# Performance work log

Hardware: AMD Instinct MI355X
Metric: run time of the kernel (lower is better)

The kernel has to match this reference:

```python
import jax, jax.numpy as jnp
import numpy as np


def setup_inputs() -> dict:
    key = jax.random.key(0)
    k1, k2, k3, k4 = jax.random.split(key, 4)
    d_in, d_out = 1024, 1024
    x = jax.random.normal(k1, (4, 2048, d_in), dtype=jnp.float32)
    # nn.Linear weights, stored as [d_in, d_out] for x @ W (torch stores transpose)
    s = 1.0 / np.sqrt(d_in)
    Wq = jax.random.normal(k2, (d_in, d_out), dtype=jnp.float32) * s
    Wk = jax.random.normal(k3, (d_in, d_out), dtype=jnp.float32) * s
    Wv = jax.random.normal(k4, (d_in, d_out), dtype=jnp.float32) * s
    return {"x": x, "Wq": Wq, "Wk": Wk, "Wv": Wv}


def reference(x, Wq, Wk, Wv):
    # x: [b, s, d_in]; projections (no bias)
    q = jnp.einsum('bsi,io->bso', x, Wq)
    k = jnp.einsum('bsi,io->bso', x, Wk)
    v = jnp.einsum('bsi,io->bso', x, Wv)
    d_out = k.shape[-1]
    scores = jnp.einsum('bqd,bkd->bqk', q, k) / jnp.sqrt(jnp.float32(d_out))
    seq_len = x.shape[1]
    causal = jnp.tril(jnp.ones((seq_len, seq_len), dtype=bool))  # [s, s]
    scores = jnp.where(causal[None, :, :], scores, -jnp.inf)
    weights = jax.nn.softmax(scores, axis=-1)
    return jnp.einsum('bqk,bkd->bqd', weights, v)
```

## Files before the change

kernel.cpp:

```cpp
#include <hip/hip_runtime.h>

typedef __attribute__((ext_vector_type(8))) short bf16x8;
typedef __attribute__((ext_vector_type(4))) float f32x4;
typedef unsigned int u32;

__device__ __forceinline__ unsigned short f2bf(float f) {
  union { float f; unsigned int u; } a; a.f = f;
  unsigned int u = a.u;
  u += 0x7FFFu + ((u >> 16) & 1u);
  return (unsigned short)(u >> 16);
}

__device__ __forceinline__ void gload16(const unsigned short* g, unsigned short* l) {
  __builtin_amdgcn_global_load_lds((const __attribute__((address_space(1))) u32*)g,
                                   (__attribute__((address_space(3))) u32*)l, 16, 0, 0);
}

#define BK 64

template<int MODE>
__global__ __launch_bounds__(256, 4)
void gemm_bt(const unsigned short* __restrict__ A,
             const unsigned short* __restrict__ Bm,
             float* __restrict__ Cf,
             float* __restrict__ Cf2,
             unsigned short* __restrict__ Cb,
             int K, long aBatch, long bBatch, long cBatch, float scale)
{
  constexpr int NI    = 2;
  constexpr int BROWS = 16;
  constexpr int BG    = 2;

  int z = blockIdx.z;
  A  += (long)z * aBatch;
  Bm += (long)z * bBatch;
  if (MODE == 2) { Cb += (long)z * cBatch; Cf += (long)z * 2048; }
  if (MODE == 3) { Cf += (long)z * cBatch; Cf2 += (long)z * 2048; }

  int bm0 = 0, bn, p = 0;
  if (MODE == 2) {
    int f = blockIdx.x;
    int r = (int)((sqrtf((float)(4 * f + 1)) - 1.0f) * 0.5f);
    while ((r + 1) * (r + 2) <= f) r++;
    while (r * (r + 1) > f) r--;
    bm0 = r * 128;
    bn  = (f - r * (r + 1)) * 64;
  } else if (MODE == 3) {
    p  = blockIdx.y;
    bn = blockIdx.x * 64;
  } else {
    bm0 = blockIdx.y * 128;
    bn  = blockIdx.x * 64;
  }

  __shared__ __align__(16) unsigned short As[128 * BK];
  __shared__ __align__(16) unsigned short Bs[64 * BK];

  int tid  = threadIdx.x;
  int wave = tid >> 6, lane = tid & 63;
  int wm = wave * 32, wn = 0;
  int quad = lane >> 4, l16 = lane & 15;

  int r8 = lane >> 3;
  int c  = (lane & 7) ^ r8;
  const unsigned short* Bg = Bm + (long)(bn + wave * BROWS + r8) * K + c * 8;
  unsigned short* Al = &As[(wave * 32) * BK];
  unsigned short* Bl = &Bs[(wave * BROWS) * BK];

  const int nseg = (MODE == 3) ? 2 : 1;
  for (int seg = 0; seg < nseg; seg++) {
    int bm   = (MODE == 3) ? ((seg == 0) ? (15 - p) * 128 : p * 128) : bm0;
    int Keff = (MODE == 3) ? ((seg == 0) ? 128 * (16 - p) : 128 * (p + 1)) : K;
    const unsigned short* Ag = A + (long)(bm + wave * 32 + r8) * K + c * 8;

    f32x4 acc[NI][4] = {};

    for (int k0 = 0; k0 < Keff; k0 += BK) {
#pragma unroll
      for (int g = 0; g < 4; g++)
        gload16(Ag + k0 + (long)g * 8 * K, Al + g * 8 * BK);
#pragma unroll
      for (int g = 0; g < BG; g++)
        gload16(Bg + k0 + (long)g * 8 * K, Bl + g * 8 * BK);
      __syncthreads();

#pragma unroll
      for (int h = 0; h < 2; h++) {
        bf16x8 af[NI], bfr[4];
#pragma unroll
        for (int i = 0; i < NI; i++)
          af[i]  = *(const bf16x8*)&As[(wm + i * 16 + l16) * BK + (((quad + 4 * h) ^ (l16 & 7)) * 8)];
#pragma unroll
        for (int j = 0; j < 4; j++)
          bfr[j] = *(const bf16x8*)&Bs[(wn + j * 16 + l16) * BK + (((quad + 4 * h) ^ (l16 & 7)) * 8)];
#pragma unroll
        for (int i = 0; i < NI; i++)
#pragma unroll
          for (int j = 0; j < 4; j++)
            acc[i][j] = __builtin_amdgcn_mfma_f32_16x16x32_bf16(af[i], bfr[j], acc[i][j], 0, 0, 0);
      }
      __syncthreads();
    }

#pragma unroll
    for (int i = 0; i < NI; i++) {
      int grow0 = bm + wm + i * 16 + quad * 4;
      if (MODE == 2) {
#pragma unroll
        for (int r = 0; r < 4; r++) {
          int grow = grow0 + r;
          float rowpart = 0.f;
#pragma unroll
          for (int j = 0; j < 4; j++) {
            int gcol = bn + j * 16 + l16;
            float e = (gcol <= grow) ? __expf(acc[i][j][r] * scale) : 0.f;
            rowpart += e;
            Cb[(long)grow * 2048 + gcol] = f2bf(e);
          }
          rowpart += __shfl_xor(rowpart, 1);
          rowpart += __shfl_xor(rowpart, 2);
          rowpart += __shfl_xor(rowpart, 4);
          rowpart += __shfl_xor(rowpart, 8);
          if (l16 == 0) atomicAdd(&Cf[grow], rowpart);
        }
      } else if (MODE == 3) {
        float rinv[4];
#pragma unroll
        for (int r = 0; r < 4; r++) rinv[r] = 1.0f / Cf2[grow0 + r];
#pragma unroll
        for (int j = 0; j < 4; j++) {
          int gcol = bn + j * 16 + l16;
#pragma unroll
          for (int r = 0; r < 4; r++)
            Cf[(long)(grow0 + r) * 1024 + gcol] = acc[i][j][r] * rinv[r];
        }
      } else {
#pragma unroll
        for (int j = 0; j < 4; j++) {
          int gcol = bn + j * 16 + l16;
#pragma unroll
          for (int r = 0; r < 4; r++)
            Cb[(long)(grow0 + r) * 1024 + gcol] = f2bf(acc[i][j][r]);
        }
      }
    }
  }
}

__global__ __launch_bounds__(512, 2)
void gemm_tv8(const unsigned short* __restrict__ A,
              const unsigned short* __restrict__ Bm,
              unsigned short* __restrict__ Cb)
{
  constexpr int NT = 16;
  constexpr int SLOT = 256 * 64;
  __shared__ __align__(16) unsigned short AsL[2 * SLOT];
  __shared__ __align__(16) unsigned short BsL[2 * SLOT];

  const int tid  = threadIdx.x;
  const int wave = tid >> 6, lane = tid & 63;
  const int quad = lane >> 4, l16 = lane & 15;
  const int wr = wave >> 2, wc = wave & 3;
  const int bm = blockIdx.y * 256;
  const int bn = blockIdx.x * 256;

  const int l8 = lane >> 3;
  const int sc = ((lane & 7) ^ l8) * 8;
  const unsigned short* Ag = A  + (long)(bm + wave * 8 + l8) * 1024 + sc;
  const unsigned short* Bg = Bm + (long)(bn + (wave >> 2) * 64 + (wave & 3) * 8 + l8) * 1024 + sc;

#define STGA(base, h, t) {                                                      \
    gload16(Ag + (long)((h) * 64) * 1024 + (t) * 64,        (base) + ((h) * 128 + wave * 8) * 64);      \
    gload16(Ag + (long)(128 + (h) * 64) * 1024 + (t) * 64,  (base) + ((h) * 128 + 64 + wave * 8) * 64); }
#define STGB(base, h, t) {                                                      \
    gload16(Bg + (long)((h) * 32) * 1024 + (t) * 64,        (base) + ((h) * 128 + wave * 8) * 64);      \
    gload16(Bg + (long)(128 + (h) * 32) * 1024 + (t) * 64,  (base) + ((h) * 128 + 64 + wave * 8) * 64); }

#define RD_A(afX, src, qm) _Pragma("unroll") for (int i = 0; i < 4; ++i)        \
    _Pragma("unroll") for (int h2 = 0; h2 < 2; ++h2)                            \
      afX[i][h2] = *(const bf16x8*)&(src)[((qm) * 128 + wr * 64 + i * 16 + l16) * 64 + (((quad + 4 * h2) ^ (l16 & 7)) * 8)];
#define RD_B(bfX, src, qn) _Pragma("unroll") for (int j = 0; j < 2; ++j)        \
    _Pragma("unroll") for (int h2 = 0; h2 < 2; ++h2)                            \
      bfX[j][h2] = *(const bf16x8*)&(src)[((qn) * 128 + wc * 32 + j * 16 + l16) * 64 + (((quad + 4 * h2) ^ (l16 & 7)) * 8)];
#define MFMA16(afX, bfX, MI0, NJ0) {                                            \
    __builtin_amdgcn_s_setprio(1);                                              \
    _Pragma("unroll") for (int i = 0; i < 4; ++i)                               \
      _Pragma("unroll") for (int j = 0; j < 2; ++j)                             \
        _Pragma("unroll") for (int h2 = 0; h2 < 2; ++h2)                        \
          acc[(MI0) + i][(NJ0) + j] =                                           \
            __builtin_amdgcn_mfma_f32_16x16x32_bf16(afX[i][h2], bfX[j][h2], acc[(MI0) + i][(NJ0) + j], 0, 0, 0); \
    __builtin_amdgcn_s_setprio(0); }

  f32x4 acc[8][4] = {};

  STGA(AsL, 0, 0) STGB(BsL, 0, 0)
  STGA(AsL, 1, 0) STGB(BsL, 1, 0)
  STGB(BsL + SLOT, 0, 1) STGA(AsL + SLOT, 1, 1)
  asm volatile("s_waitcnt vmcnt(4)" ::: "memory");
  __builtin_amdgcn_sched_barrier(0);
  __builtin_amdgcn_s_barrier();

#pragma unroll 1
  for (int u = 0; u < NT; ++u) {
    const int b = u & 1;
    const unsigned short* Asb = AsL + b * SLOT;
    const unsigned short* Bsb = BsL + b * SLOT;
    unsigned short* Asn = AsL + (b ^ 1) * SLOT;
    unsigned short* Bsn = BsL + (b ^ 1) * SLOT;
    unsigned short* Asc = AsL + b * SLOT;
    unsigned short* Bsc = BsL + b * SLOT;

    bf16x8 af0[4][2], af1[4][2], bf0[2][2], bf1[2][2];

    RD_A(af0, Asb, 0)
    RD_B(bf0, Bsb, 0)
    if (u + 1 < NT) { STGA(Asn, 0, u + 1) STGB(Bsn, 1, u + 1) }
    __builtin_amdgcn_s_barrier();
    MFMA16(af0, bf0, 0, 0)
    __builtin_amdgcn_s_barrier();

    RD_A(af1, Asb, 1)
    if (u + 2 < NT) STGB(Bsc, 0, u + 2)
    __builtin_amdgcn_s_barrier();
    MFMA16(af1, bf0, 4, 0)
    __builtin_amdgcn_s_barrier();

    RD_B(bf1, Bsb, 1)
    if (u + 2 < NT) STGA(Asc, 1, u + 2)
    __builtin_amdgcn_s_barrier();
    MFMA16(af1, bf1, 4, 2)
    __builtin_amdgcn_s_barrier();

    if (u < NT - 2)       { asm volatile("s_waitcnt vmcnt(4)" ::: "memory"); }
    else if (u == NT - 2) { asm volatile("s_waitcnt vmcnt(0)" ::: "memory"); }
    __builtin_amdgcn_sched_barrier(0);
    __builtin_amdgcn_s_barrier();
    MFMA16(af0, bf1, 0, 2)
    __builtin_amdgcn_s_barrier();
  }
#undef STGA
#undef STGB
#undef RD_A
#undef RD_B
#undef MFMA16

#pragma unroll
  for (int mi = 0; mi < 8; ++mi) {
    int grow0 = bm + wr * 128 + mi * 16 + quad * 4;
#pragma unroll
    for (int nj = 0; nj < 4; ++nj) {
      int gcol = bn + wc * 64 + nj * 16 + l16;
      int which = gcol >> 10;
      int col = gcol & 1023;
      if (which == 0) {
#pragma unroll
        for (int r = 0; r < 4; r++)
          Cb[(long)(grow0 + r) * 1024 + col] = f2bf(acc[mi][nj][r]);
      } else {
        unsigned short* Vt = Cb + (long)8192 * 1024;
        int bb = grow0 >> 11, s = grow0 & 2047;
        ushort4 pk;
        pk.x = f2bf(acc[mi][nj][0]); pk.y = f2bf(acc[mi][nj][1]);
        pk.z = f2bf(acc[mi][nj][2]); pk.w = f2bf(acc[mi][nj][3]);
        *(ushort4*)(Vt + ((long)bb * 1024 + col) * 2048 + s) = pk;
      }
    }
  }
}

__global__ __launch_bounds__(256)
void prep(const float* __restrict__ x,
          const float* __restrict__ W0, const float* __restrict__ W1,
          const float* __restrict__ W2,
          unsigned short* __restrict__ Xb,
          unsigned short* __restrict__ Wqb, unsigned short* __restrict__ Wkb,
          unsigned short* __restrict__ WvT,
          float* __restrict__ rsum)
{
  __shared__ float tile[32][33];
  int b = blockIdx.x;
  if (b < 8192) {
    long i = ((long)b * 256 + threadIdx.x) * 4;
    float4 v = *(const float4*)(x + i);
    ushort4 o;
    o.x = f2bf(v.x); o.y = f2bf(v.y); o.z = f2bf(v.z); o.w = f2bf(v.w);
    *(ushort4*)(Xb + i) = o;
  } else if (b < 10240) {
    int t = b - 8192;
    const float* W    = (t < 1024) ? W0 : W1;
    unsigned short* D = (t < 1024) ? Wqb : Wkb;
    long i = ((long)(t & 1023) * 256 + threadIdx.x) * 4;
    float4 v = *(const float4*)(W + i);
    ushort4 o;
    o.x = f2bf(v.x); o.y = f2bf(v.y); o.z = f2bf(v.z); o.w = f2bf(v.w);
    *(ushort4*)(D + i) = o;
  } else if (b < 11264) {
    int q = b - 10240;
    int kb = (q >> 5) * 32, nb = (q & 31) * 32;
    int tx = threadIdx.x & 31, ty = threadIdx.x >> 5;
    for (int r = ty; r < 32; r += 8)
      tile[r][tx] = W2[(long)(kb + r) * 1024 + nb + tx];
    __syncthreads();
    for (int r = ty; r < 32; r += 8)
      WvT[(long)(nb + r) * 1024 + kb + tx] = f2bf(tile[tx][r]);
  } else {
    long i = ((long)(b - 11264) * 256 + threadIdx.x) * 4;
    float4 zz = {0.f, 0.f, 0.f, 0.f};
    *(float4*)(rsum + i) = zz;
  }
}

extern "C" void kernel_launch(void* const* d_in, const int* in_sizes, int n_in,
                              void* d_out, int out_size, void* d_ws, size_t ws_size,
                              hipStream_t stream) {
  const float* x  = (const float*)d_in[0];
  const float* Wq = (const float*)d_in[1];
  const float* Wk = (const float*)d_in[2];
  const float* Wv = (const float*)d_in[3];
  float* out = (float*)d_out;

  unsigned short* Xb  = (unsigned short*)d_ws;
  unsigned short* Wqb = Xb  + (long)8192 * 1024;
  unsigned short* Wkb = Wqb + (long)1024 * 1024;
  unsigned short* TVB = Wkb + (long)1024 * 1024;
  unsigned short* T   = TVB + (long)2048 * 1024;
  unsigned short* Vt  = T   + (long)8192 * 1024;
  unsigned short* E   = Vt  + (long)8192 * 1024;
  float* rsum         = (float*)(E + (long)4 * 2048 * 2048);

  prep<<<11272, 256, 0, stream>>>(x, Wq, Wk, Wv, Xb, Wqb, Wkb,
                                  TVB + (long)1024 * 1024, rsum);

  gemm_bt<1><<<dim3(16, 8, 1), 256, 0, stream>>>(Wkb, Wqb, nullptr, nullptr, TVB,
      1024, 0, 0, 0, 1.f);

  gemm_tv8<<<dim3(8, 32, 1), 512, 0, stream>>>(Xb, TVB, T);

  gemm_bt<2><<<dim3(272, 1, 4), 256, 0, stream>>>(T, Xb, rsum, nullptr, E, 1024,
      (long)2048 * 1024, (long)2048 * 1024, (long)2048 * 2048, 0.03125f);

  gemm_bt<3><<<dim3(16, 8, 4), 256, 0, stream>>>(E, Vt, out, rsum, nullptr, 2048,
      (long)2048 * 2048, (long)1024 * 2048, (long)2048 * 1024, 1.f);
}
```

Baseline: 217.1 us.

## Fuse Wk·Wqᵀ weight GEMM into prep kernel, converting fp32 to bf16 on load

The separate Wq/Wk bf16 conversion pass and the gemm_bt<1> launch that computed Wk·Wqᵀ are replaced by 128 extra blocks in the prep kernel. Each block reads fp32 weights directly, converts them to bf16 into swizzled LDS, and runs MFMA to write TVB. This removes one kernel launch and the round trip through intermediate bf16 weight buffers. The cost is an unpipelined, smaller GEMM tile inside a kernel that also does elementwise work, which could lengthen the critical path if those 128 blocks are slow.

```diff
diff --git a/kernel.cpp b/kernel.cpp
--- a/kernel.cpp
+++ b/kernel.cpp
@@ -134,14 +134,6 @@
           for (int r = 0; r < 4; r++)
             Cf[(long)(grow0 + r) * 1024 + gcol] = acc[i][j][r] * rinv[r];
         }
-      } else {
-#pragma unroll
-        for (int j = 0; j < 4; j++) {
-          int gcol = bn + j * 16 + l16;
-#pragma unroll
-          for (int r = 0; r < 4; r++)
-            Cb[(long)(grow0 + r) * 1024 + gcol] = f2bf(acc[i][j][r]);
-        }
       }
     }
   }
@@ -269,42 +261,104 @@
 }
 
 __global__ __launch_bounds__(256)
-void prep(const float* __restrict__ x,
-          const float* __restrict__ W0, const float* __restrict__ W1,
-          const float* __restrict__ W2,
-          unsigned short* __restrict__ Xb,
-          unsigned short* __restrict__ Wqb, unsigned short* __restrict__ Wkb,
-          unsigned short* __restrict__ WvT,
-          float* __restrict__ rsum)
+void prep_mt(const float* __restrict__ x,
+             const float* __restrict__ Wqf, const float* __restrict__ Wkf,
+             const float* __restrict__ Wvf,
+             unsigned short* __restrict__ Xb,
+             unsigned short* __restrict__ TVB,
+             float* __restrict__ rsum)
 {
+  __shared__ __align__(16) unsigned short As[128 * 64];
+  __shared__ __align__(16) unsigned short Bs[64 * 64];
   __shared__ float tile[32][33];
-  int b = blockIdx.x;
-  if (b < 8192) {
-    long i = ((long)b * 256 + threadIdx.x) * 4;
+  int b = blockIdx.x, tid = threadIdx.x;
+
+  if (b < 128) {
+    int bm = (b >> 4) * 128, bn = (b & 15) * 64;
+    int wave = tid >> 6, lane = tid & 63;
+    int quad = lane >> 4, l16 = lane & 15;
+    int r8 = lane >> 3, cc = lane & 7;
+    int csrc = (cc ^ r8) * 8;
+    f32x4 acc[2][4] = {};
+
+    for (int k0 = 0; k0 < 1024; k0 += 64) {
+#pragma unroll
+      for (int g = 0; g < 4; g++) {
+        int lrow = wave * 32 + g * 8 + r8;
+        const float* s = Wkf + (long)(bm + lrow) * 1024 + k0 + csrc;
+        float4 v0 = *(const float4*)s, v1 = *(const float4*)(s + 4);
+        bf16x8 o;
+        o[0] = (short)f2bf(v0.x); o[1] = (short)f2bf(v0.y);
+        o[2] = (short)f2bf(v0.z); o[3] = (short)f2bf(v0.w);
+        o[4] = (short)f2bf(v1.x); o[5] = (short)f2bf(v1.y);
+        o[6] = (short)f2bf(v1.z); o[7] = (short)f2bf(v1.w);
+        *(bf16x8*)&As[lrow * 64 + cc * 8] = o;
+      }
+#pragma unroll
+      for (int g = 0; g < 2; g++) {
+        int lrow = wave * 16 + g * 8 + r8;
+        const float* s = Wqf + (long)(bn + lrow) * 1024 + k0 + csrc;
+        float4 v0 = *(const float4*)s, v1 = *(const float4*)(s + 4);
+        bf16x8 o;
+        o[0] = (short)f2bf(v0.x); o[1] = (short)f2bf(v0.y);
+        o[2] = (short)f2bf(v0.z); o[3] = (short)f2bf(v0.w);
+        o[4] = (short)f2bf(v1.x); o[5] = (short)f2bf(v1.y);
+        o[6] = (short)f2bf(v1.z); o[7] = (short)f2bf(v1.w);
+        *(bf16x8*)&Bs[lrow * 64 + cc * 8] = o;
+      }
+      __syncthreads();
+
+#pragma unroll
+      for (int h = 0; h < 2; h++) {
+        bf16x8 af[2], bfr[4];
+#pragma unroll
+        for (int i = 0; i < 2; i++)
+          af[i]  = *(const bf16x8*)&As[(wave * 32 + i * 16 + l16) * 64 + (((quad + 4 * h) ^ (l16 & 7)) * 8)];
+#pragma unroll
+        for (int j = 0; j < 4; j++)
+          bfr[j] = *(const bf16x8*)&Bs[(j * 16 + l16) * 64 + (((quad + 4 * h) ^ (l16 & 7)) * 8)];
+#pragma unroll
+        for (int i = 0; i < 2; i++)
+#pragma unroll
+          for (int j = 0; j < 4; j++)
+            acc[i][j] = __builtin_amdgcn_mfma_f32_16x16x32_bf16(af[i], bfr[j], acc[i][j], 0, 0, 0);
+      }
+      __syncthreads();
+    }
+
+#pragma unroll
+    for (int i = 0; i < 2; i++) {
+      int grow0 = bm + wave * 32 + i * 16 + quad * 4;
+#pragma unroll
+      for (int j = 0; j < 4; j++) {
+        int gcol = bn + j * 16 + l16;
+#pragma unroll
+        for (int r = 0; r < 4; r++)
+          TVB[(long)(grow0 + r) * 1024 + gcol] = f2bf(acc[i][j][r]);
+      }
+    }
+    return;
+  }
+
+  int b2 = b - 128;
+  if (b2 < 8192) {
+    long i = ((long)b2 * 256 + tid) * 4;
     float4 v = *(const float4*)(x + i);
     ushort4 o;
     o.x = f2bf(v.x); o.y = f2bf(v.y); o.z = f2bf(v.z); o.w = f2bf(v.w);
     *(ushort4*)(Xb + i) = o;
-  } else if (b < 10240) {
-    int t = b - 8192;
-    const float* W    = (t < 1024) ? W0 : W1;
-    unsigned short* D = (t < 1024) ? Wqb : Wkb;
-    long i = ((long)(t & 1023) * 256 + threadIdx.x) * 4;
-    float4 v = *(const float4*)(W + i);
-    ushort4 o;
-    o.x = f2bf(v.x); o.y = f2bf(v.y); o.z = f2bf(v.z); o.w = f2bf(v.w);
-    *(ushort4*)(D + i) = o;
-  } else if (b < 11264) {
-    int q = b - 10240;
+  } else if (b2 < 9216) {
+    unsigned short* WvT = TVB + (long)1024 * 1024;
+    int q = b2 - 8192;
     int kb = (q >> 5) * 32, nb = (q & 31) * 32;
-    int tx = threadIdx.x & 31, ty = threadIdx.x >> 5;
+    int tx = tid & 31, ty = tid >> 5;
     for (int r = ty; r < 32; r += 8)
-      tile[r][tx] = W2[(long)(kb + r) * 1024 + nb + tx];
+      tile[r][tx] = Wvf[(long)(kb + r) * 1024 + nb + tx];
     __syncthreads();
     for (int r = ty; r < 32; r += 8)
       WvT[(long)(nb + r) * 1024 + kb + tx] = f2bf(tile[tx][r]);
   } else {
-    long i = ((long)(b - 11264) * 256 + threadIdx.x) * 4;
+    long i = ((long)(b2 - 9216) * 256 + tid) * 4;
     float4 zz = {0.f, 0.f, 0.f, 0.f};
     *(float4*)(rsum + i) = zz;
   }
@@ -320,19 +374,13 @@
   float* out = (float*)d_out;
 
   unsigned short* Xb  = (unsigned short*)d_ws;
-  unsigned short* Wqb = Xb  + (long)8192 * 1024;
-  unsigned short* Wkb = Wqb + (long)1024 * 1024;
-  unsigned short* TVB = Wkb + (long)1024 * 1024;
+  unsigned short* TVB = Xb + (long)8192 * 1024 + (long)2 * 1024 * 1024;
   unsigned short* T   = TVB + (long)2048 * 1024;
   unsigned short* Vt  = T   + (long)8192 * 1024;
   unsigned short* E   = Vt  + (long)8192 * 1024;
   float* rsum         = (float*)(E + (long)4 * 2048 * 2048);
 
-  prep<<<11272, 256, 0, stream>>>(x, Wq, Wk, Wv, Xb, Wqb, Wkb,
-                                  TVB + (long)1024 * 1024, rsum);
-
-  gemm_bt<1><<<dim3(16, 8, 1), 256, 0, stream>>>(Wkb, Wqb, nullptr, nullptr, TVB,
-      1024, 0, 0, 0, 1.f);
+  prep_mt<<<9352, 256, 0, stream>>>(x, Wq, Wk, Wv, Xb, TVB, rsum);
 
   gemm_tv8<<<dim3(8, 32, 1), 512, 0, stream>>>(Xb, TVB, T);
 
```

New measurement: 233.2 us. 7.4% more time.
